# Performance work log

Measured on AMD Instinct MI355X. Metric: run time of the kernel, lower is better.

## Reference

```python
import jax, jax.numpy as jnp
import numpy as np


def setup_inputs() -> dict:
    key = jax.random.key(0)
    k1, k2, k3, k4, k5, k6 = jax.random.split(key, 6)
    B, T, U, D, V = 4, 512, 128, 512, 512
    speech = jax.random.normal(k1, (B, T, D), dtype=jnp.float32)
    text = jax.random.normal(k2, (B, U, D), dtype=jnp.float32)
    W = jax.random.normal(k3, (V, D), dtype=jnp.float32) / np.sqrt(D)
    b = jax.random.normal(k4, (V,), dtype=jnp.float32) * 0.01
    speech_len = jax.random.randint(k5, (B,), 1, T + 1, dtype=jnp.int32)
    text_len = jax.random.randint(k6, (B,), 1, U + 1, dtype=jnp.int32)
    return {"speech": speech, "text": text, "W": W, "b": b,
            "speech_len": speech_len, "text_len": text_len}


def reference(speech, text, W, b, speech_len, text_len):
    # RNN-T joint network: broadcast-add encoder and predictor outputs,
    # then project to vocab. speech: [B,T,D], text: [B,U,D].
    joint = speech[:, :, None, :] + text[:, None, :, :]       # [B,T,U,D]
    logits = jnp.einsum('btud,vd->btuv', joint, W) + b         # [B,T,U,V]
    return logits, speech_len, text_len
```

## Files before the change

### kernel.cpp

```cpp
#include <hip/hip_runtime.h>

#define B_ 4
#define T_ 512
#define U_ 128
#define D_ 512
#define V_ 512
#define MS (B_ * T_)
#define MT (B_ * U_)
#define MTOT (MS + MT)
#define LOGITS_ELEMS ((size_t)B_ * T_ * U_ * V_)

#define TILE 64
#define TILE_K 32
#define LDS_STRIDE 36

__global__ __launch_bounds__(256, 2) void gemm_joint(
    const float* __restrict__ speech, const float* __restrict__ text,
    const float* __restrict__ W, const float* __restrict__ bias,
    float* __restrict__ S, float* __restrict__ Tx)
{
    __shared__ float Xs[TILE * LDS_STRIDE];
    __shared__ float Ws[TILE * LDS_STRIDE];

    const int tid = threadIdx.x;
    const int m0 = blockIdx.x * TILE;
    const int n0 = blockIdx.y * TILE;
    const int tx = tid & 15;
    const int ty = tid >> 4;

    float acc[4][4] = {};

    for (int k0 = 0; k0 < D_; k0 += TILE_K) {
        #pragma unroll
        for (int i = 0; i < 2; ++i) {
            const int f4  = tid + i * 256;
            const int row = f4 >> 3;
            const int col = (f4 & 7) * 4;
            const int m = m0 + row;
            const float* src = (m < MS) ? (speech + (size_t)m * D_)
                                        : (text + (size_t)(m - MS) * D_);
            *(float4*)(&Xs[row * LDS_STRIDE + col]) =
                *(const float4*)(src + k0 + col);
            *(float4*)(&Ws[row * LDS_STRIDE + col]) =
                *(const float4*)(W + (size_t)(n0 + row) * D_ + k0 + col);
        }
        __syncthreads();

        #pragma unroll
        for (int kk = 0; kk < TILE_K; kk += 4) {
            float4 a[4], b[4];
            #pragma unroll
            for (int i = 0; i < 4; ++i)
                a[i] = *(const float4*)(&Xs[(ty * 4 + i) * LDS_STRIDE + kk]);
            #pragma unroll
            for (int j = 0; j < 4; ++j)
                b[j] = *(const float4*)(&Ws[(tx * 4 + j) * LDS_STRIDE + kk]);
            #pragma unroll
            for (int i = 0; i < 4; ++i) {
                #pragma unroll
                for (int j = 0; j < 4; ++j) {
                    acc[i][j] += a[i].x * b[j].x;
                    acc[i][j] += a[i].y * b[j].y;
                    acc[i][j] += a[i].z * b[j].z;
                    acc[i][j] += a[i].w * b[j].w;
                }
            }
        }
        __syncthreads();
    }

    const int vbase = n0 + tx * 4;
    #pragma unroll
    for (int i = 0; i < 4; ++i) {
        const int m = m0 + ty * 4 + i;
        float4 o;
        o.x = acc[i][0]; o.y = acc[i][1]; o.z = acc[i][2]; o.w = acc[i][3];
        if (m < MS) {
            *(float4*)(S + (size_t)m * V_ + vbase) = o;
        } else {
            o.x += bias[vbase + 0];
            o.y += bias[vbase + 1];
            o.z += bias[vbase + 2];
            o.w += bias[vbase + 3];
            *(float4*)(Tx + (size_t)(m - MS) * V_ + vbase) = o;
        }
    }
}

__global__ __launch_bounds__(256) void bcast_add(
    const float* __restrict__ S, const float* __restrict__ Tx,
    float* __restrict__ out)
{
    const int V4 = V_ / 4;
    const int bt = blockIdx.x;
    const int b  = bt >> 9;
    const int tid = threadIdx.x;

    const float4* S4 = (const float4*)S + (size_t)bt * V4;
    const float4* T4 = (const float4*)Tx + (size_t)b * U_ * V4;
    float4* O4 = (float4*)out + (size_t)bt * U_ * V4;

    const float4 sv = S4[tid & (V4 - 1)];

    #pragma unroll 4
    for (int idx = tid; idx < U_ * V4; idx += 256) {
        float4 tv = T4[idx];
        float4 o;
        o.x = sv.x + tv.x;
        o.y = sv.y + tv.y;
        o.z = sv.z + tv.z;
        o.w = sv.w + tv.w;
        O4[idx] = o;
    }
}

__global__ void copy_lens(const int* __restrict__ sl, const int* __restrict__ tl,
                          float* __restrict__ out)
{
    const int i = threadIdx.x;
    if (i < B_)            out[LOGITS_ELEMS + i] = (float)sl[i];
    else if (i < 2 * B_)   out[LOGITS_ELEMS + i] = (float)tl[i - B_];
}

extern "C" void kernel_launch(void* const* d_in, const int* in_sizes, int n_in,
                              void* d_out, int out_size, void* d_ws, size_t ws_size,
                              hipStream_t stream) {
    const float* speech = (const float*)d_in[0];
    const float* text   = (const float*)d_in[1];
    const float* W      = (const float*)d_in[2];
    const float* bias   = (const float*)d_in[3];
    const int*   sl     = (const int*)d_in[4];
    const int*   tl     = (const int*)d_in[5];
    float* out = (float*)d_out;

    float* S  = (float*)d_ws;
    float* Tx = S + (size_t)MS * V_;

    dim3 g1(MTOT / TILE, V_ / TILE);
    gemm_joint<<<g1, 256, 0, stream>>>(speech, text, W, bias, S, Tx);

    bcast_add<<<MS, 256, 0, stream>>>(S, Tx, out);

    copy_lens<<<1, 64, 0, stream>>>(sl, tl, out);
}
```

Before: 643.1 us.

## Retile GEMM with register prefetch, nontemporal broadcast stores, fold length copy

The GEMM switches to 128x64 tiles stored k-major in LDS, and prefetches the next K tile into registers while the current one is being computed. The broadcast-add kernel uses nontemporal stores for the large logits output and has a larger unroll. The separate copy_lens kernel is merged into the broadcast kernel, which removes one launch. Runtime is dominated by the roughly 537MB output write, so the GEMM changes matter little; nontemporal stores may help write bandwidth.

```diff
diff --git a/kernel.cpp b/kernel.cpp
--- a/kernel.cpp
+++ b/kernel.cpp
@@ -10,69 +10,114 @@
 #define MTOT (MS + MT)
 #define LOGITS_ELEMS ((size_t)B_ * T_ * U_ * V_)
 
-#define TILE 64
-#define TILE_K 32
-#define LDS_STRIDE 36
+#define TM 128
+#define TN 64
+#define TK 32
+#define NTILES (D_ / TK)
+#define XSTR 132
+#define WSTR 68
+
+typedef float f32x4 __attribute__((ext_vector_type(4)));
 
 __global__ __launch_bounds__(256, 2) void gemm_joint(
     const float* __restrict__ speech, const float* __restrict__ text,
     const float* __restrict__ W, const float* __restrict__ bias,
     float* __restrict__ S, float* __restrict__ Tx)
 {
-    __shared__ float Xs[TILE * LDS_STRIDE];
-    __shared__ float Ws[TILE * LDS_STRIDE];
+    __shared__ float Xt[TK][XSTR];
+    __shared__ float Wt[TK][WSTR];
 
     const int tid = threadIdx.x;
-    const int m0 = blockIdx.x * TILE;
-    const int n0 = blockIdx.y * TILE;
+    const int m0 = blockIdx.x * TM;
+    const int n0 = blockIdx.y * TN;
     const int tx = tid & 15;
     const int ty = tid >> 4;
 
-    float acc[4][4] = {};
+    const float* xbase = (m0 < MS) ? (speech + (size_t)m0 * D_)
+                                   : (text + (size_t)(m0 - MS) * D_);
 
-    for (int k0 = 0; k0 < D_; k0 += TILE_K) {
-        #pragma unroll
-        for (int i = 0; i < 2; ++i) {
-            const int f4  = tid + i * 256;
-            const int row = f4 >> 3;
-            const int col = (f4 & 7) * 4;
-            const int m = m0 + row;
-            const float* src = (m < MS) ? (speech + (size_t)m * D_)
-                                        : (text + (size_t)(m - MS) * D_);
-            *(float4*)(&Xs[row * LDS_STRIDE + col]) =
-                *(const float4*)(src + k0 + col);
-            *(float4*)(&Ws[row * LDS_STRIDE + col]) =
-                *(const float4*)(W + (size_t)(n0 + row) * D_ + k0 + col);
-        }
-        __syncthreads();
+    float acc[8][4] = {};
+    float4 xr[4], wr[2];
 
-        #pragma unroll
-        for (int kk = 0; kk < TILE_K; kk += 4) {
-            float4 a[4], b[4];
-            #pragma unroll
-            for (int i = 0; i < 4; ++i)
-                a[i] = *(const float4*)(&Xs[(ty * 4 + i) * LDS_STRIDE + kk]);
-            #pragma unroll
-            for (int j = 0; j < 4; ++j)
-                b[j] = *(const float4*)(&Ws[(tx * 4 + j) * LDS_STRIDE + kk]);
+    #pragma unroll
+    for (int i = 0; i < 4; ++i) {
+        const int q = tid + 256 * i;
+        xr[i] = *(const float4*)(xbase + (size_t)(q >> 3) * D_ + ((q & 7) << 2));
+    }
+    #pragma unroll
+    for (int i = 0; i < 2; ++i) {
+        const int q = tid + 256 * i;
+        wr[i] = *(const float4*)(W + (size_t)(n0 + (q >> 3)) * D_ + ((q & 7) << 2));
+    }
+    #pragma unroll
+    for (int i = 0; i < 4; ++i) {
+        const int q = tid + 256 * i;
+        const int r = q >> 3, c = (q & 7) << 2;
+        Xt[c + 0][r] = xr[i].x; Xt[c + 1][r] = xr[i].y;
+        Xt[c + 2][r] = xr[i].z; Xt[c + 3][r] = xr[i].w;
+    }
+    #pragma unroll
+    for (int i = 0; i < 2; ++i) {
+        const int q = tid + 256 * i;
+        const int r = q >> 3, c = (q & 7) << 2;
+        Wt[c + 0][r] = wr[i].x; Wt[c + 1][r] = wr[i].y;
+        Wt[c + 2][r] = wr[i].z; Wt[c + 3][r] = wr[i].w;
+    }
+    __syncthreads();
+
+    for (int t = 0; t < NTILES; ++t) {
+        if (t + 1 < NTILES) {
+            const int kn = (t + 1) * TK;
             #pragma unroll
             for (int i = 0; i < 4; ++i) {
-                #pragma unroll
-                for (int j = 0; j < 4; ++j) {
-                    acc[i][j] += a[i].x * b[j].x;
-                    acc[i][j] += a[i].y * b[j].y;
-                    acc[i][j] += a[i].z * b[j].z;
-                    acc[i][j] += a[i].w * b[j].w;
-                }
+                const int q = tid + 256 * i;
+                xr[i] = *(const float4*)(xbase + (size_t)(q >> 3) * D_ + kn + ((q & 7) << 2));
+            }
+            #pragma unroll
+            for (int i = 0; i < 2; ++i) {
+                const int q = tid + 256 * i;
+                wr[i] = *(const float4*)(W + (size_t)(n0 + (q >> 3)) * D_ + kn + ((q & 7) << 2));
             }
         }
-        __syncthreads();
+
+        #pragma unroll 8
+        for (int k = 0; k < TK; ++k) {
+            const float4 a0 = *(const float4*)&Xt[k][ty * 8];
+            const float4 a1 = *(const float4*)&Xt[k][ty * 8 + 4];
+            const float4 b0 = *(const float4*)&Wt[k][tx * 4];
+            const float av[8] = {a0.x, a0.y, a0.z, a0.w, a1.x, a1.y, a1.z, a1.w};
+            const float bv[4] = {b0.x, b0.y, b0.z, b0.w};
+            #pragma unroll
+            for (int i = 0; i < 8; ++i)
+                #pragma unroll
+                for (int j = 0; j < 4; ++j)
+                    acc[i][j] += av[i] * bv[j];
+        }
+
+        if (t + 1 < NTILES) {
+            __syncthreads();
+            #pragma unroll
+            for (int i = 0; i < 4; ++i) {
+                const int q = tid + 256 * i;
+                const int r = q >> 3, c = (q & 7) << 2;
+                Xt[c + 0][r] = xr[i].x; Xt[c + 1][r] = xr[i].y;
+                Xt[c + 2][r] = xr[i].z; Xt[c + 3][r] = xr[i].w;
+            }
+            #pragma unroll
+            for (int i = 0; i < 2; ++i) {
+                const int q = tid + 256 * i;
+                const int r = q >> 3, c = (q & 7) << 2;
+                Wt[c + 0][r] = wr[i].x; Wt[c + 1][r] = wr[i].y;
+                Wt[c + 2][r] = wr[i].z; Wt[c + 3][r] = wr[i].w;
+            }
+            __syncthreads();
+        }
     }
 
     const int vbase = n0 + tx * 4;
     #pragma unroll
-    for (int i = 0; i < 4; ++i) {
-        const int m = m0 + ty * 4 + i;
+    for (int i = 0; i < 8; ++i) {
+        const int m = m0 + ty * 8 + i;
         float4 o;
         o.x = acc[i][0]; o.y = acc[i][1]; o.z = acc[i][2]; o.w = acc[i][3];
         if (m < MS) {
@@ -87,8 +132,9 @@
     }
 }
 
-__global__ __launch_bounds__(256) void bcast_add(
+__global__ __launch_bounds__(256, 8) void bcast_add(
     const float* __restrict__ S, const float* __restrict__ Tx,
+    const int* __restrict__ sl, const int* __restrict__ tl,
     float* __restrict__ out)
 {
     const int V4 = V_ / 4;
@@ -96,30 +142,22 @@
     const int b  = bt >> 9;
     const int tid = threadIdx.x;
 
-    const float4* S4 = (const float4*)S + (size_t)bt * V4;
-    const float4* T4 = (const float4*)Tx + (size_t)b * U_ * V4;
-    float4* O4 = (float4*)out + (size_t)bt * U_ * V4;
+    if (bt == 0 && tid < 2 * B_) {
+        out[LOGITS_ELEMS + tid] = (tid < B_) ? (float)sl[tid]
+                                             : (float)tl[tid - B_];
+    }
 
-    const float4 sv = S4[tid & (V4 - 1)];
+    const f32x4* S4 = (const f32x4*)S + (size_t)bt * V4;
+    const f32x4* T4 = (const f32x4*)Tx + (size_t)b * U_ * V4;
+    f32x4* O4 = (f32x4*)out + (size_t)bt * U_ * V4;
 
-    #pragma unroll 4
+    const f32x4 sv = S4[tid & (V4 - 1)];
+
+    #pragma unroll 8
     for (int idx = tid; idx < U_ * V4; idx += 256) {
-        float4 tv = T4[idx];
-        float4 o;
-        o.x = sv.x + tv.x;
-        o.y = sv.y + tv.y;
-        o.z = sv.z + tv.z;
-        o.w = sv.w + tv.w;
-        O4[idx] = o;
+        const f32x4 tv = T4[idx];
+        __builtin_nontemporal_store(sv + tv, &O4[idx]);
     }
-}
-
-__global__ void copy_lens(const int* __restrict__ sl, const int* __restrict__ tl,
-                          float* __restrict__ out)
-{
-    const int i = threadIdx.x;
-    if (i < B_)            out[LOGITS_ELEMS + i] = (float)sl[i];
-    else if (i < 2 * B_)   out[LOGITS_ELEMS + i] = (float)tl[i - B_];
 }
 
 extern "C" void kernel_launch(void* const* d_in, const int* in_sizes, int n_in,
@@ -136,10 +174,8 @@
     float* S  = (float*)d_ws;
     float* Tx = S + (size_t)MS * V_;
 
-    dim3 g1(MTOT / TILE, V_ / TILE);
+    dim3 g1(MTOT / TM, V_ / TN);
     gemm_joint<<<g1, 256, 0, stream>>>(speech, text, W, bias, S, Tx);
 
-    bcast_add<<<MS, 256, 0, stream>>>(S, Tx, out);
-
-    copy_lens<<<1, 64, 0, stream>>>(sl, tl, out);
+    bcast_add<<<MS, 256, 0, stream>>>(S, Tx, sl, tl, out);
 }
```

Result: faster. 573.8 us (-10.8%).
